# Kernel tuning notes

Measured on AMD Instinct MI355X. Metric: run time of the kernel, lower is better.

Reference implementation:

```python
import jax, jax.numpy as jnp
import numpy as np

NUM_CLIENTS = 4
ACT_K = 2
B, N, C_IN, C_OUT, D = 32, 2048, 64, 64, 8
NPC = N // NUM_CLIENTS  # nodes per client (contiguous partition, matching args.nodes_per)


def kron_rows(A, B_):
    # torch.cartesian_prod per row then product == row-wise Kronecker product
    return (A[:, :, None] * B_[:, None, :]).reshape(A.shape[0], -1)


def transform(k, E):
    # exponentiation-by-squaring of row-wise Kronecker powers: E^{(x)k}, shape [N, D**k]
    t = jnp.ones((E.shape[0], 1), E.dtype)
    cur = E
    while k > 0:
        if k % 2 == 1:
            t = kron_rows(t, cur)
        cur = kron_rows(cur, cur)
        k //= 2
    return t


def setup_inputs() -> dict:
    key = jax.random.key(0)
    k0, k1, k2, k3, k4 = jax.random.split(key, 5)
    return {
        "x": jax.random.normal(k0, (B, N, C_IN), dtype=jnp.float32),
        "node_embeddings": jax.random.normal(k1, (N, D), dtype=jnp.float32),
        "poly_coefficients": jax.random.normal(k2, (NUM_CLIENTS, 1, ACT_K + 1), dtype=jnp.float32),
        "mask": jnp.ones((B, N, C_IN), dtype=jnp.float32),
        "weights_pool": jax.random.normal(k3, (NUM_CLIENTS, D, C_IN, C_OUT), dtype=jnp.float32) * 0.1,
        "bias_pool": jax.random.normal(k4, (NUM_CLIENTS, D, C_OUT), dtype=jnp.float32) * 0.1,
    }


def reference(x, node_embeddings, poly_coefficients, mask, weights_pool, bias_pool):
    H = x * mask                                   # [B,N,C]
    E = node_embeddings                            # [N,D]
    TE = [transform(i, E) for i in range(ACT_K + 1)]          # widths D**i
    EH = [jnp.einsum('ne,bnc->bec', t, H) for t in TE]         # [B, D**i, C]

    # sparsity (sp) over per-client partial aggregates
    Hg = H.reshape(B, NUM_CLIENTS, NPC, C_IN)
    num = jnp.float32(0.0); den = 0.0
    for t in TE:
        tg = t.reshape(NUM_CLIENTS, NPC, -1)
        cl = jnp.einsum('gne,bgnc->gbec', tg, Hg)  # per-client EH
        num = num + jnp.count_nonzero(cl).astype(jnp.float32)
        den = den + float(cl.size)
    sp = 1.0 - num / (den + 1e-10)

    # transmission stat (tran) over full aggregates
    num2 = jnp.float32(0.0); den2 = 0.0
    for eh in EH:
        num2 = num2 + jnp.count_nonzero(eh).astype(jnp.float32)
        den2 = den2 + float(eh.size)
    tran = (1.0 - sp + num2 / (den2 + 1e-10)) / 2.0

    # adaptive polynomial aggregation: Z_k = TE_k @ EH_k, combined by per-client poly coeffs
    Z = jnp.stack([jnp.einsum('ne,bec->bnc', TE[i], EH[i]) for i in range(ACT_K + 1)])  # [K,B,N,C]
    Zg = Z.reshape(ACT_K + 1, B, NUM_CLIENTS, NPC, C_IN)
    Zp = jnp.einsum('gk,kbgnc->bgnc', poly_coefficients[:, 0, :], Zg).reshape(B, N, C_IN)
    Z = H + Zp                                     # residual

    # node-adaptive weights/bias per client, then per-node GEMM (gather-MLP-scatter)
    Eg = E.reshape(NUM_CLIENTS, NPC, D)
    W = jnp.einsum('gnd,gdio->gnio', Eg, weights_pool)   # [G,NPC,C_in,C_out]
    bvec = jnp.einsum('gnd,gdo->gno', Eg, bias_pool)     # [G,NPC,C_out]
    Zc = Z.reshape(B, NUM_CLIENTS, NPC, C_IN)
    out = jnp.einsum('bgni,gnio->bgno', Zc, W) + bvec[None]
    ret = out.reshape(B, N, C_OUT)  # contiguous nodes_per => scatter by indices is identity
    return (ret, sp, tran)
```

## Files before the change

kernel.cpp:

```cpp
#include <hip/hip_runtime.h>
#include <hip/hip_bf16.h>

#define NC   4
#define BB   32
#define NN   2048
#define CI   64
#define CO   64
#define DD   8
#define NPCL 512
#define EW   73
#define CHN  128

template<int LO, int CNT>
__device__ __forceinline__ void k1_body(const float (*H_lds)[CI],
                                        const float (*E_lds)[DD],
                                        int c, float* __restrict__ part_out) {
  float acc[CNT];
#pragma unroll
  for (int k = 0; k < CNT; ++k) acc[k] = 0.f;

#pragma unroll 4
  for (int n = 0; n < CHN; ++n) {
    float4 e0 = *reinterpret_cast<const float4*>(&E_lds[n][0]);
    float4 e1 = *reinterpret_cast<const float4*>(&E_lds[n][4]);
    float ev[8];
    ev[0] = e0.x; ev[1] = e0.y; ev[2] = e0.z; ev[3] = e0.w;
    ev[4] = e1.x; ev[5] = e1.y; ev[6] = e1.z; ev[7] = e1.w;
    const float h = H_lds[n][c];
    float evh[8];
#pragma unroll
    for (int d = 0; d < 8; ++d) evh[d] = ev[d] * h;
#pragma unroll
    for (int k = 0; k < CNT; ++k) {
      const int e = LO + k;
      if (e == 0) acc[k] += h;
      else if (e < 9) acc[k] += evh[e - 1];
      else {
        const int r = e - 9;
        acc[k] = fmaf(ev[r >> 3], evh[r & 7], acc[k]);
      }
    }
  }
#pragma unroll
  for (int k = 0; k < CNT; ++k) part_out[(LO + k) * CI + c] = acc[k];
}

__global__ __launch_bounds__(256) void k1_partial(
    const float* __restrict__ x, const float* __restrict__ mask,
    const float* __restrict__ E, float* __restrict__ part) {
  __shared__ float H_lds[CHN][CI];
  __shared__ float E_lds[CHN][DD];
  const int bid = blockIdx.x;
  const int g = bid >> 7;
  const int b = (bid >> 2) & 31;
  const int p = bid & 3;
  const int n0 = g * NPCL + p * CHN;
  const int tid = threadIdx.x;

  {
    const float4* xp = reinterpret_cast<const float4*>(x + ((size_t)b * NN + n0) * CI);
    const float4* mp = reinterpret_cast<const float4*>(mask + ((size_t)b * NN + n0) * CI);
    float4* hl = reinterpret_cast<float4*>(&H_lds[0][0]);
    for (int i = tid; i < CHN * CI / 4; i += 256) {
      float4 xv = xp[i], mv = mp[i];
      xv.x *= mv.x; xv.y *= mv.y; xv.z *= mv.z; xv.w *= mv.w;
      hl[i] = xv;
    }
    const float4* ep = reinterpret_cast<const float4*>(E + (size_t)n0 * DD);
    float4* el = reinterpret_cast<float4*>(&E_lds[0][0]);
    if (tid < CHN * DD / 4) el[tid] = ep[tid];
  }
  __syncthreads();

  const int c = tid & 63;
  const int q = tid >> 6;
  float* pp = part + (size_t)bid * (EW * CI);
  switch (q) {
    case 0: k1_body<0, 19>(H_lds, E_lds, c, pp); break;
    case 1: k1_body<19, 18>(H_lds, E_lds, c, pp); break;
    case 2: k1_body<37, 18>(H_lds, E_lds, c, pp); break;
    default: k1_body<55, 18>(H_lds, E_lds, c, pp); break;
  }
}

__global__ __launch_bounds__(256) void k2_reduce(
    const float* __restrict__ part, float* __restrict__ EH,
    unsigned int* __restrict__ cnt) {
  const int tid = threadIdx.x;
  const int i = blockIdx.x * 256 + tid;
  const int b = i / (EW * CI);
  const int ec = i - b * (EW * CI);

  float s = 0.f;
  int c1 = 0;
#pragma unroll
  for (int g = 0; g < 4; ++g) {
    float cl = 0.f;
#pragma unroll
    for (int p = 0; p < 4; ++p)
      cl += part[(size_t)(((g * 32 + b) * 4 + p)) * (EW * CI) + ec];
    c1 += (cl != 0.f) ? 1 : 0;
    s += cl;
  }
  const int c2 = (s != 0.f) ? 1 : 0;
  EH[i] = s;

  __shared__ int r1[256], r2[256];
  r1[tid] = c1; r2[tid] = c2;
  __syncthreads();
  for (int st = 128; st > 0; st >>= 1) {
    if (tid < st) { r1[tid] += r1[tid + st]; r2[tid] += r2[tid + st]; }
    __syncthreads();
  }
  if (tid == 0) {
    atomicAdd(&cnt[0], (unsigned int)r1[0]);
    atomicAdd(&cnt[1], (unsigned int)r2[0]);
  }
}

__global__ void k2_scalars(const unsigned int* __restrict__ cnt,
                           float* __restrict__ out_scalars) {
  const float num  = (float)cnt[0];
  const float num2 = (float)cnt[1];
  const float den  = (float)(598016.0 + 1e-10);
  const float den2 = (float)(149504.0 + 1e-10);
  const float sp   = 1.0f - num / den;
  const float r2   = num2 / den2;
  const float tran = (1.0f - sp + r2) * 0.5f;
  out_scalars[0] = sp;
  out_scalars[1] = tran;
}

__global__ __launch_bounds__(256) void k3_out(
    const float* __restrict__ x, const float* __restrict__ mask,
    const float* __restrict__ E, const float* __restrict__ poly,
    const float* __restrict__ Wp, const float* __restrict__ bp,
    const float* __restrict__ EH, float* __restrict__ out) {
  __shared__ float tep[4][EW];
  __shared__ float Ee[4][8];
  __shared__ float Z_lds[4][32][66];
  __shared__ float W_lds[64][64];

  const int nb = blockIdx.x * 4;
  const int g = nb >> 9;
  const int tid = threadIdx.x;

  if (tid < 32) Ee[tid >> 3][tid & 7] = E[(size_t)(nb + (tid >> 3)) * DD + (tid & 7)];
  __syncthreads();

  const float p0 = poly[g * 3 + 0];
  const float p1 = poly[g * 3 + 1];
  const float p2 = poly[g * 3 + 2];
  for (int idx = tid; idx < 4 * EW; idx += 256) {
    const int nd = idx / EW, e = idx - nd * EW;
    float te, pk;
    if (e == 0) { te = 1.f; pk = p0; }
    else if (e < 9) { te = Ee[nd][e - 1]; pk = p1; }
    else { const int r = e - 9; te = Ee[nd][r >> 3] * Ee[nd][r & 7]; pk = p2; }
    tep[nd][e] = te * pk;
  }
  __syncthreads();

  const int b = tid >> 3;
  const int c0 = (tid & 7) * 8;
  float acc[4][8];
#pragma unroll
  for (int nd = 0; nd < 4; ++nd) {
    const float* xp = x + ((size_t)b * NN + nb + nd) * CI + c0;
    const float* mp = mask + ((size_t)b * NN + nb + nd) * CI + c0;
    float4 x0 = *reinterpret_cast<const float4*>(xp);
    float4 x1 = *reinterpret_cast<const float4*>(xp + 4);
    float4 m0 = *reinterpret_cast<const float4*>(mp);
    float4 m1 = *reinterpret_cast<const float4*>(mp + 4);
    acc[nd][0] = x0.x * m0.x; acc[nd][1] = x0.y * m0.y;
    acc[nd][2] = x0.z * m0.z; acc[nd][3] = x0.w * m0.w;
    acc[nd][4] = x1.x * m1.x; acc[nd][5] = x1.y * m1.y;
    acc[nd][6] = x1.z * m1.z; acc[nd][7] = x1.w * m1.w;
  }
  const float* ehb = EH + (size_t)b * (EW * CI) + c0;
  for (int e = 0; e < EW; ++e) {
    float4 h0 = *reinterpret_cast<const float4*>(ehb + e * CI);
    float4 h1 = *reinterpret_cast<const float4*>(ehb + e * CI + 4);
    float eh[8];
    eh[0] = h0.x; eh[1] = h0.y; eh[2] = h0.z; eh[3] = h0.w;
    eh[4] = h1.x; eh[5] = h1.y; eh[6] = h1.z; eh[7] = h1.w;
#pragma unroll
    for (int nd = 0; nd < 4; ++nd) {
      const float t = tep[nd][e];
#pragma unroll
      for (int j = 0; j < 8; ++j) acc[nd][j] += t * eh[j];
    }
  }
#pragma unroll
  for (int nd = 0; nd < 4; ++nd)
#pragma unroll
    for (int j = 0; j < 8; ++j)
      Z_lds[nd][b][c0 + j] = acc[nd][j];
  __syncthreads();

  const int o0 = (tid & 7) * 8;
  for (int nd = 0; nd < 4; ++nd) {
    for (int idx = tid; idx < 64 * 64; idx += 256) {
      const int i = idx >> 6, o = idx & 63;
      float w = 0.f;
#pragma unroll
      for (int d = 0; d < 8; ++d)
        w += Ee[nd][d] * Wp[((size_t)(g * 8 + d) * 64 + i) * 64 + o];
      W_lds[i][o] = w;
    }
    __syncthreads();

    float ob[8];
#pragma unroll
    for (int j = 0; j < 8; ++j) {
      float bv = 0.f;
#pragma unroll
      for (int d = 0; d < 8; ++d)
        bv += Ee[nd][d] * bp[(size_t)(g * 8 + d) * 64 + o0 + j];
      ob[j] = bv;
    }
    for (int i = 0; i < 64; ++i) {
      const float z = Z_lds[nd][b][i];
      float4 w0 = *reinterpret_cast<const float4*>(&W_lds[i][o0]);
      float4 w1 = *reinterpret_cast<const float4*>(&W_lds[i][o0 + 4]);
      ob[0] += z * w0.x; ob[1] += z * w0.y; ob[2] += z * w0.z; ob[3] += z * w0.w;
      ob[4] += z * w1.x; ob[5] += z * w1.y; ob[6] += z * w1.z; ob[7] += z * w1.w;
    }
    float* op = out + ((size_t)b * NN + nb + nd) * CO + o0;
    *reinterpret_cast<float4*>(op) = make_float4(ob[0], ob[1], ob[2], ob[3]);
    *reinterpret_cast<float4*>(op + 4) = make_float4(ob[4], ob[5], ob[6], ob[7]);
    __syncthreads();
  }
}

extern "C" void kernel_launch(void* const* d_in, const int* in_sizes, int n_in,
                              void* d_out, int out_size, void* d_ws, size_t ws_size,
                              hipStream_t stream) {
  const float* x    = (const float*)d_in[0];
  const float* E    = (const float*)d_in[1];
  const float* poly = (const float*)d_in[2];
  const float* mask = (const float*)d_in[3];
  const float* Wp   = (const float*)d_in[4];
  const float* bp   = (const float*)d_in[5];
  float* out = (float*)d_out;

  char* ws = (char*)d_ws;
  float* part = (float*)ws;
  float* EH   = (float*)(ws + 9568256);
  unsigned int* cnt = (unsigned int*)(ws + 9568256 + 598016);

  hipMemsetAsync(cnt, 0, 2 * sizeof(unsigned int), stream);
  k1_partial<<<512, 256, 0, stream>>>(x, mask, E, part);
  k2_reduce<<<584, 256, 0, stream>>>(part, EH, cnt);
  k2_scalars<<<1, 1, 0, stream>>>(cnt, out + (size_t)BB * NN * CO);
  k3_out<<<512, 256, 0, stream>>>(x, mask, E, poly, Wp, bp, EH, out);
}
```

Before: 91.74 us.

## Split output stage into Z kernel and bf16 MFMA GEMM over node-adaptive weights

The fused output kernel is replaced by three kernels. A preprocessing kernel converts the weight pool to a transposed bf16 layout and precomputes per-node biases. A Z kernel computes the polynomial aggregation plus residual and stores Z as bf16. A GEMM kernel uses MFMA 16x16x32 bf16 instructions per embedding dimension and combines the partial results with per-node embedding scalars, which avoids materialising a separate W per node. This removes the repeated per-node W construction and the scalar FMA GEMM, at the cost of bf16 precision loss on Z and W, extra launches, and a Z round-trip through memory.

```diff
diff --git a/kernel.cpp b/kernel.cpp
--- a/kernel.cpp
+++ b/kernel.cpp
@@ -10,6 +10,14 @@
 #define NPCL 512
 #define EW   73
 #define CHN  128
+
+typedef __attribute__((ext_vector_type(8))) short bf16x8;
+typedef __attribute__((ext_vector_type(4))) float f32x4;
+
+__device__ __forceinline__ unsigned int rne_bf16(float f) {
+  unsigned int b = __float_as_uint(f);
+  return (b + 0x7FFFu + ((b >> 16) & 1u)) >> 16;
+}
 
 template<int LO, int CNT>
 __device__ __forceinline__ void k1_body(const float (*H_lds)[CI],
@@ -131,106 +139,209 @@
   out_scalars[1] = tran;
 }
 
-__global__ __launch_bounds__(256) void k3_out(
+__global__ __launch_bounds__(256) void k0_pre(
+    const float* __restrict__ Wp, const float* __restrict__ bp,
+    const float* __restrict__ E,
+    unsigned short* __restrict__ Wpt, float* __restrict__ bvec) {
+  const int idx = blockIdx.x * 256 + threadIdx.x;
+  if (idx < 131072) {
+    const int g = idx >> 15, rem = idx & 32767;
+    const int o = rem >> 9, k = rem & 511, d = k >> 6, i = k & 63;
+    Wpt[idx] = (unsigned short)rne_bf16(Wp[((size_t)(g * 8 + d) * 64 + i) * 64 + o]);
+  } else {
+    const int j = idx - 131072;
+    const int n = j >> 6, o = j & 63, g = n >> 9;
+    float s = 0.f;
+#pragma unroll
+    for (int d = 0; d < 8; ++d)
+      s = fmaf(E[(size_t)n * 8 + d], bp[(size_t)(g * 8 + d) * 64 + o], s);
+    bvec[j] = s;
+  }
+}
+
+__global__ __launch_bounds__(256) void k3a_z(
     const float* __restrict__ x, const float* __restrict__ mask,
     const float* __restrict__ E, const float* __restrict__ poly,
-    const float* __restrict__ Wp, const float* __restrict__ bp,
-    const float* __restrict__ EH, float* __restrict__ out) {
-  __shared__ float tep[4][EW];
-  __shared__ float Ee[4][8];
-  __shared__ float Z_lds[4][32][66];
-  __shared__ float W_lds[64][64];
-
-  const int nb = blockIdx.x * 4;
-  const int g = nb >> 9;
+    const float* __restrict__ EH, unsigned short* __restrict__ Zb) {
+  __shared__ float EH_s[EW][64];
+  __shared__ float tep_s[64][EW];
+  __shared__ float E_s[64][8];
+
+  const int blk = blockIdx.x;
+  const int b  = blk >> 5;
+  const int n0 = (blk & 31) << 6;
+  const int g  = n0 >> 9;
   const int tid = threadIdx.x;
 
-  if (tid < 32) Ee[tid >> 3][tid & 7] = E[(size_t)(nb + (tid >> 3)) * DD + (tid & 7)];
-  __syncthreads();
-
-  const float p0 = poly[g * 3 + 0];
-  const float p1 = poly[g * 3 + 1];
-  const float p2 = poly[g * 3 + 2];
-  for (int idx = tid; idx < 4 * EW; idx += 256) {
-    const int nd = idx / EW, e = idx - nd * EW;
+  if (tid < 128) {
+    const int row = tid >> 1, h = tid & 1;
+    *(float4*)&E_s[row][h * 4] = *(const float4*)&E[(size_t)(n0 + row) * 8 + h * 4];
+  }
+  {
+    const float4* src = (const float4*)(EH + (size_t)b * (EW * 64));
+    float4* dst = (float4*)&EH_s[0][0];
+    for (int i = tid; i < EW * 16; i += 256) dst[i] = src[i];
+  }
+  __syncthreads();
+
+  const float p0 = poly[g * 3 + 0], p1 = poly[g * 3 + 1], p2 = poly[g * 3 + 2];
+  for (int idx = tid; idx < 64 * EW; idx += 256) {
+    const int nd = idx & 63, e = idx >> 6;
     float te, pk;
     if (e == 0) { te = 1.f; pk = p0; }
-    else if (e < 9) { te = Ee[nd][e - 1]; pk = p1; }
-    else { const int r = e - 9; te = Ee[nd][r >> 3] * Ee[nd][r & 7]; pk = p2; }
-    tep[nd][e] = te * pk;
-  }
-  __syncthreads();
-
-  const int b = tid >> 3;
+    else if (e < 9) { te = E_s[nd][e - 1]; pk = p1; }
+    else { const int r = e - 9; te = E_s[nd][r >> 3] * E_s[nd][r & 7]; pk = p2; }
+    tep_s[nd][e] = te * pk;
+  }
+  __syncthreads();
+
   const int c0 = (tid & 7) * 8;
-  float acc[4][8];
-#pragma unroll
-  for (int nd = 0; nd < 4; ++nd) {
-    const float* xp = x + ((size_t)b * NN + nb + nd) * CI + c0;
-    const float* mp = mask + ((size_t)b * NN + nb + nd) * CI + c0;
-    float4 x0 = *reinterpret_cast<const float4*>(xp);
-    float4 x1 = *reinterpret_cast<const float4*>(xp + 4);
-    float4 m0 = *reinterpret_cast<const float4*>(mp);
-    float4 m1 = *reinterpret_cast<const float4*>(mp + 4);
-    acc[nd][0] = x0.x * m0.x; acc[nd][1] = x0.y * m0.y;
-    acc[nd][2] = x0.z * m0.z; acc[nd][3] = x0.w * m0.w;
-    acc[nd][4] = x1.x * m1.x; acc[nd][5] = x1.y * m1.y;
-    acc[nd][6] = x1.z * m1.z; acc[nd][7] = x1.w * m1.w;
-  }
-  const float* ehb = EH + (size_t)b * (EW * CI) + c0;
+  const int ndl = tid >> 3;
+  float acc[2][8];
+#pragma unroll
+  for (int u = 0; u < 2; ++u) {
+    const int n = n0 + ndl + u * 32;
+    const float4* xp = (const float4*)(x + ((size_t)b * NN + n) * CI + c0);
+    const float4* mp = (const float4*)(mask + ((size_t)b * NN + n) * CI + c0);
+    float4 x0 = xp[0], x1 = xp[1], m0 = mp[0], m1 = mp[1];
+    acc[u][0] = x0.x * m0.x; acc[u][1] = x0.y * m0.y;
+    acc[u][2] = x0.z * m0.z; acc[u][3] = x0.w * m0.w;
+    acc[u][4] = x1.x * m1.x; acc[u][5] = x1.y * m1.y;
+    acc[u][6] = x1.z * m1.z; acc[u][7] = x1.w * m1.w;
+  }
+#pragma unroll 1
   for (int e = 0; e < EW; ++e) {
-    float4 h0 = *reinterpret_cast<const float4*>(ehb + e * CI);
-    float4 h1 = *reinterpret_cast<const float4*>(ehb + e * CI + 4);
-    float eh[8];
-    eh[0] = h0.x; eh[1] = h0.y; eh[2] = h0.z; eh[3] = h0.w;
-    eh[4] = h1.x; eh[5] = h1.y; eh[6] = h1.z; eh[7] = h1.w;
-#pragma unroll
-    for (int nd = 0; nd < 4; ++nd) {
-      const float t = tep[nd][e];
-#pragma unroll
-      for (int j = 0; j < 8; ++j) acc[nd][j] += t * eh[j];
-    }
-  }
-#pragma unroll
-  for (int nd = 0; nd < 4; ++nd)
-#pragma unroll
-    for (int j = 0; j < 8; ++j)
-      Z_lds[nd][b][c0 + j] = acc[nd][j];
-  __syncthreads();
-
-  const int o0 = (tid & 7) * 8;
-  for (int nd = 0; nd < 4; ++nd) {
-    for (int idx = tid; idx < 64 * 64; idx += 256) {
-      const int i = idx >> 6, o = idx & 63;
-      float w = 0.f;
-#pragma unroll
-      for (int d = 0; d < 8; ++d)
-        w += Ee[nd][d] * Wp[((size_t)(g * 8 + d) * 64 + i) * 64 + o];
-      W_lds[i][o] = w;
-    }
-    __syncthreads();
-
-    float ob[8];
-#pragma unroll
-    for (int j = 0; j < 8; ++j) {
-      float bv = 0.f;
-#pragma unroll
-      for (int d = 0; d < 8; ++d)
-        bv += Ee[nd][d] * bp[(size_t)(g * 8 + d) * 64 + o0 + j];
-      ob[j] = bv;
-    }
-    for (int i = 0; i < 64; ++i) {
-      const float z = Z_lds[nd][b][i];
-      float4 w0 = *reinterpret_cast<const float4*>(&W_lds[i][o0]);
-      float4 w1 = *reinterpret_cast<const float4*>(&W_lds[i][o0 + 4]);
-      ob[0] += z * w0.x; ob[1] += z * w0.y; ob[2] += z * w0.z; ob[3] += z * w0.w;
-      ob[4] += z * w1.x; ob[5] += z * w1.y; ob[6] += z * w1.z; ob[7] += z * w1.w;
-    }
-    float* op = out + ((size_t)b * NN + nb + nd) * CO + o0;
-    *reinterpret_cast<float4*>(op) = make_float4(ob[0], ob[1], ob[2], ob[3]);
-    *reinterpret_cast<float4*>(op + 4) = make_float4(ob[4], ob[5], ob[6], ob[7]);
-    __syncthreads();
-  }
+    float4 h0 = *(const float4*)&EH_s[e][c0];
+    float4 h1 = *(const float4*)&EH_s[e][c0 + 4];
+    const float t0 = tep_s[ndl][e];
+    const float t1 = tep_s[ndl + 32][e];
+    acc[0][0] = fmaf(t0, h0.x, acc[0][0]); acc[0][1] = fmaf(t0, h0.y, acc[0][1]);
+    acc[0][2] = fmaf(t0, h0.z, acc[0][2]); acc[0][3] = fmaf(t0, h0.w, acc[0][3]);
+    acc[0][4] = fmaf(t0, h1.x, acc[0][4]); acc[0][5] = fmaf(t0, h1.y, acc[0][5]);
+    acc[0][6] = fmaf(t0, h1.z, acc[0][6]); acc[0][7] = fmaf(t0, h1.w, acc[0][7]);
+    acc[1][0] = fmaf(t1, h0.x, acc[1][0]); acc[1][1] = fmaf(t1, h0.y, acc[1][1]);
+    acc[1][2] = fmaf(t1, h0.z, acc[1][2]); acc[1][3] = fmaf(t1, h0.w, acc[1][3]);
+    acc[1][4] = fmaf(t1, h1.x, acc[1][4]); acc[1][5] = fmaf(t1, h1.y, acc[1][5]);
+    acc[1][6] = fmaf(t1, h1.z, acc[1][6]); acc[1][7] = fmaf(t1, h1.w, acc[1][7]);
+  }
+#pragma unroll
+  for (int u = 0; u < 2; ++u) {
+    unsigned int w[4];
+#pragma unroll
+    for (int q = 0; q < 4; ++q) {
+      unsigned int lo = rne_bf16(acc[u][2 * q]);
+      unsigned int hb = __float_as_uint(acc[u][2 * q + 1]);
+      unsigned int hi = (hb + 0x7FFFu + ((hb >> 16) & 1u)) & 0xFFFF0000u;
+      w[q] = hi | lo;
+    }
+    const int n = n0 + ndl + u * 32;
+    *(uint4*)(Zb + ((size_t)b * NN + n) * CI + c0) = *(uint4*)w;
+  }
+}
+
+__global__ __launch_bounds__(256) void k3b_gemm(
+    const unsigned short* __restrict__ Zb,
+    const unsigned short* __restrict__ Wpt,
+    const float* __restrict__ E,
+    const float* __restrict__ bvec,
+    float* __restrict__ out) {
+  __shared__ unsigned short Z_lds[128][72];
+  __shared__ unsigned short Bt[2][64][40];
+  __shared__ float E_lds[128][8];
+
+  const int blk = blockIdx.x;
+  const int b  = blk >> 4;
+  const int n0 = (blk & 15) << 7;
+  const int g  = n0 >> 9;
+  const int tid = threadIdx.x;
+  const int wave = tid >> 6;
+  const int lane = tid & 63;
+  const int l15 = lane & 15;
+  const int kg  = lane >> 4;
+  const int wrow = wave * 32;
+
+  {
+    const int row = tid >> 1, half = tid & 1;
+    const bf16x8* src = (const bf16x8*)(Zb + ((size_t)b * NN + n0 + row) * CI + half * 32);
+    bf16x8* dst = (bf16x8*)&Z_lds[row][half * 32];
+#pragma unroll
+    for (int q = 0; q < 4; ++q) dst[q] = src[q];
+  }
+  {
+    const int row = tid >> 1, h = tid & 1;
+    *(float4*)&E_lds[row][h * 4] = *(const float4*)&E[(size_t)(n0 + row) * 8 + h * 4];
+  }
+  const int so = tid >> 2, skq = tid & 3;
+  *(bf16x8*)&Bt[0][so][skq * 8] =
+      *(const bf16x8*)(Wpt + ((size_t)g * 64 + so) * 512 + skq * 8);
+  __syncthreads();
+
+  f32x4 fin[2][4];
+#pragma unroll
+  for (int i = 0; i < 2; ++i)
+#pragma unroll
+    for (int j = 0; j < 4; ++j) fin[i][j] = (f32x4){0.f, 0.f, 0.f, 0.f};
+  const f32x4 zf = (f32x4){0.f, 0.f, 0.f, 0.f};
+
+  for (int d = 0; d < 8; ++d) {
+    f32x4 tmp[2][4];
+#pragma unroll
+    for (int st = 0; st < 2; ++st) {
+      const int s = d * 2 + st;
+      bf16x8 nxt;
+      if (s < 15)
+        nxt = *(const bf16x8*)(Wpt + ((size_t)g * 64 + so) * 512 + (s + 1) * 32 + skq * 8);
+      const int buf = s & 1;
+      bf16x8 a0 = *(const bf16x8*)&Z_lds[wrow + l15][st * 32 + kg * 8];
+      bf16x8 a1 = *(const bf16x8*)&Z_lds[wrow + 16 + l15][st * 32 + kg * 8];
+      bf16x8 b0 = *(const bf16x8*)&Bt[buf][l15][kg * 8];
+      bf16x8 b1 = *(const bf16x8*)&Bt[buf][l15 + 16][kg * 8];
+      bf16x8 b2 = *(const bf16x8*)&Bt[buf][l15 + 32][kg * 8];
+      bf16x8 b3 = *(const bf16x8*)&Bt[buf][l15 + 48][kg * 8];
+      if (st == 0) {
+        tmp[0][0] = __builtin_amdgcn_mfma_f32_16x16x32_bf16(a0, b0, zf, 0, 0, 0);
+        tmp[0][1] = __builtin_amdgcn_mfma_f32_16x16x32_bf16(a0, b1, zf, 0, 0, 0);
+        tmp[0][2] = __builtin_amdgcn_mfma_f32_16x16x32_bf16(a0, b2, zf, 0, 0, 0);
+        tmp[0][3] = __builtin_amdgcn_mfma_f32_16x16x32_bf16(a0, b3, zf, 0, 0, 0);
+        tmp[1][0] = __builtin_amdgcn_mfma_f32_16x16x32_bf16(a1, b0, zf, 0, 0, 0);
+        tmp[1][1] = __builtin_amdgcn_mfma_f32_16x16x32_bf16(a1, b1, zf, 0, 0, 0);
+        tmp[1][2] = __builtin_amdgcn_mfma_f32_16x16x32_bf16(a1, b2, zf, 0, 0, 0);
+        tmp[1][3] = __builtin_amdgcn_mfma_f32_16x16x32_bf16(a1, b3, zf, 0, 0, 0);
+      } else {
+        tmp[0][0] = __builtin_amdgcn_mfma_f32_16x16x32_bf16(a0, b0, tmp[0][0], 0, 0, 0);
+        tmp[0][1] = __builtin_amdgcn_mfma_f32_16x16x32_bf16(a0, b1, tmp[0][1], 0, 0, 0);
+        tmp[0][2] = __builtin_amdgcn_mfma_f32_16x16x32_bf16(a0, b2, tmp[0][2], 0, 0, 0);
+        tmp[0][3] = __builtin_amdgcn_mfma_f32_16x16x32_bf16(a0, b3, tmp[0][3], 0, 0, 0);
+        tmp[1][0] = __builtin_amdgcn_mfma_f32_16x16x32_bf16(a1, b0, tmp[1][0], 0, 0, 0);
+        tmp[1][1] = __builtin_amdgcn_mfma_f32_16x16x32_bf16(a1, b1, tmp[1][1], 0, 0, 0);
+        tmp[1][2] = __builtin_amdgcn_mfma_f32_16x16x32_bf16(a1, b2, tmp[1][2], 0, 0, 0);
+        tmp[1][3] = __builtin_amdgcn_mfma_f32_16x16x32_bf16(a1, b3, tmp[1][3], 0, 0, 0);
+      }
+      if (s < 15) *(bf16x8*)&Bt[buf ^ 1][so][skq * 8] = nxt;
+      __syncthreads();
+    }
+#pragma unroll
+    for (int rf = 0; rf < 2; ++rf)
+#pragma unroll
+      for (int j = 0; j < 4; ++j) {
+        const float ev = E_lds[wrow + rf * 16 + kg * 4 + j][d];
+#pragma unroll
+        for (int cf = 0; cf < 4; ++cf)
+          fin[rf][cf][j] = fmaf(ev, tmp[rf][cf][j], fin[rf][cf][j]);
+      }
+  }
+
+#pragma unroll
+  for (int rf = 0; rf < 2; ++rf)
+#pragma unroll
+    for (int j = 0; j < 4; ++j) {
+      const int n = n0 + wrow + rf * 16 + kg * 4 + j;
+      const float* bv = bvec + (size_t)n * 64 + l15;
+      float* op = out + ((size_t)b * NN + n) * CO + l15;
+#pragma unroll
+      for (int cf = 0; cf < 4; ++cf)
+        op[cf * 16] = fin[rf][cf][j] + bv[cf * 16];
+    }
 }
 
 extern "C" void kernel_launch(void* const* d_in, const int* in_sizes, int n_in,
@@ -245,13 +356,18 @@
   float* out = (float*)d_out;
 
   char* ws = (char*)d_ws;
-  float* part = (float*)ws;
-  float* EH   = (float*)(ws + 9568256);
-  unsigned int* cnt = (unsigned int*)(ws + 9568256 + 598016);
+  float* part          = (float*)ws;
+  unsigned short* Zb   = (unsigned short*)ws;
+  unsigned short* Wpt  = (unsigned short*)(ws + 8388608);
+  float* bvec          = (float*)(ws + 8650752);
+  float* EH            = (float*)(ws + 9568256);
+  unsigned int* cnt    = (unsigned int*)(ws + 10166272);
 
   hipMemsetAsync(cnt, 0, 2 * sizeof(unsigned int), stream);
   k1_partial<<<512, 256, 0, stream>>>(x, mask, E, part);
   k2_reduce<<<584, 256, 0, stream>>>(part, EH, cnt);
   k2_scalars<<<1, 1, 0, stream>>>(cnt, out + (size_t)BB * NN * CO);
-  k3_out<<<512, 256, 0, stream>>>(x, mask, E, poly, Wp, bp, EH, out);
-}
+  k0_pre<<<1024, 256, 0, stream>>>(Wp, bp, E, Wpt, bvec);
+  k3a_z<<<1024, 256, 0, stream>>>(x, mask, E, poly, EH, Zb);
+  k3b_gemm<<<512, 256, 0, stream>>>(Zb, Wpt, E, bvec, out);
+}
```

Result: faster. 87.69 us (-4.4%).
